# Performance work log

Hardware: AMD Instinct MI355X
Metric: run time of the kernel (lower is better)

## Reference

```python
import jax, jax.numpy as jnp
import numpy as np
from jax import lax

B, T, H, W, D = 4, 24, 32, 32, 128
N_CONV = 5            # 32 -> 1 via five stride-2 convs
NUM_FREQS = T // 2    # 12
N_EXPERTS = 7         # unique int periods of rfftfreq(24)[1:]
TOP_K = 2
BN_EPS = 1e-5
COMBINE_EPS = float(np.finfo(np.float64).eps)


def setup_inputs() -> dict:
    key = jax.random.key(0)
    ks = jax.random.split(key, 12)
    x = jax.random.normal(ks[0], (B, T, H, W, D), jnp.float32)
    conv_w = jax.random.normal(ks[1], (N_CONV, D, D, 2, 2), jnp.float32) / np.sqrt(4 * D)
    conv_b = jax.random.normal(ks[2], (N_CONV, D), jnp.float32) * 0.1
    bn_gamma = jax.random.uniform(ks[3], (N_CONV, D), jnp.float32, 0.5, 1.5)
    bn_beta = jax.random.normal(ks[4], (N_CONV, D), jnp.float32) * 0.1
    bn_mean = jax.random.normal(ks[5], (N_CONV, D), jnp.float32) * 0.1
    bn_var = jax.random.uniform(ks[6], (N_CONV, D), jnp.float32, 0.5, 1.5)
    fuse_w = jax.random.normal(ks[7], (D, 1), jnp.float32) / np.sqrt(D)
    fuse_b = jax.random.normal(ks[8], (1,), jnp.float32) * 0.1
    w_gate = jax.random.normal(ks[9], (NUM_FREQS, N_EXPERTS), jnp.float32)
    expert_w = jax.random.normal(ks[10], (N_EXPERTS, D, D), jnp.float32) / np.sqrt(D)
    expert_b = jax.random.normal(ks[11], (N_EXPERTS, D), jnp.float32) * 0.1
    return dict(x=x, conv_w=conv_w, conv_b=conv_b, bn_gamma=bn_gamma, bn_beta=bn_beta,
                bn_mean=bn_mean, bn_var=bn_var, fuse_w=fuse_w, fuse_b=fuse_b,
                w_gate=w_gate, expert_w=expert_w, expert_b=expert_b, top_k=TOP_K)


def _gates(x, conv_w, conv_b, bn_gamma, bn_beta, bn_mean, bn_var, fuse_w, fuse_b, w_gate, top_k):
    b, t, h, w, d = x.shape
    # (b t h w d) -> (bt, d, h, w)
    z = jnp.transpose(x.reshape(b * t, h, w, d), (0, 3, 1, 2))
    for i in range(conv_w.shape[0]):  # fixed small layer loop
        z = lax.conv_general_dilated(z, conv_w[i], (2, 2), 'VALID',
                                     dimension_numbers=('NCHW', 'OIHW', 'NCHW'))
        z = z + conv_b[i][None, :, None, None]
        z = bn_gamma[i][None, :, None, None] * (z - bn_mean[i][None, :, None, None]) \
            * lax.rsqrt(bn_var[i][None, :, None, None] + BN_EPS) + bn_beta[i][None, :, None, None]
        z = jnp.where(z > 0, z, 0.2 * z)  # LeakyReLU(0.2)
    hh, ww = z.shape[-2], z.shape[-1]
    # (bt, d, h, w) -> (b, t, h*w*d)  matching einops '(b t) d h w -> b t (h w d)'
    z = jnp.transpose(z.reshape(b, t, d, hh, ww), (0, 1, 3, 4, 2)).reshape(b, t, hh * ww * d)
    s = (z @ fuse_w + fuse_b)[..., 0]  # [B, T]
    xf = jnp.fft.rfft(s, axis=-1, norm='ortho')[:, 1:]  # drop DC -> [B, T//2]
    amp = jnp.abs(xf)
    logits = amp @ w_gate  # [B, E]  (eval path: no noise)
    top_vals, top_idx = lax.top_k(logits, top_k + 1)
    tk_vals, tk_idx = top_vals[:, :top_k], top_idx[:, :top_k]
    tk_gates = jax.nn.softmax(tk_vals, axis=-1)
    gates = jnp.zeros_like(logits).at[jnp.arange(b)[:, None], tk_idx].set(tk_gates)
    return gates


def reference(x, conv_w, conv_b, bn_gamma, bn_beta, bn_mean, bn_var,
              fuse_w, fuse_b, w_gate, expert_w, expert_b, top_k):
    gates = _gates(x, conv_w, conv_b, bn_gamma, bn_beta, bn_mean, bn_var,
                   fuse_w, fuse_b, w_gate, top_k)  # [B, E]
    # Dense equivalent of dispatch -> per-expert linear -> combine:
    # combine does exp(expert_out), gate-weighted scatter-add over batch, then log.
    expert_out = jnp.einsum('bthwd,edf->bethwf', x, expert_w) \
                 + expert_b[None, :, None, None, None, :]  # [B,E,T,H,W,D]
    combined = jnp.einsum('be,bethwf->bthwf', gates, jnp.exp(expert_out))
    combined = jnp.where(combined == 0, COMBINE_EPS, combined)
    return jnp.log(combined)
```

## Files before the change

### kernel.cpp

```cpp
#include <hip/hip_runtime.h>
#include <hip/hip_bf16.h>

#define D_ 128
#define T_ 24
#define NPB 24576
#define TSTR 132

typedef __attribute__((ext_vector_type(8))) short bf16x8;
typedef __attribute__((ext_vector_type(4))) float f32x4;
typedef unsigned short ushortt;

static __device__ __forceinline__ void load8(const float* p, float* dst){
  float4 a = *(const float4*)p; float4 b = *(const float4*)(p+4);
  dst[0]=a.x;dst[1]=a.y;dst[2]=a.z;dst[3]=a.w;dst[4]=b.x;dst[5]=b.y;dst[6]=b.z;dst[7]=b.w;
}
static __device__ __forceinline__ bf16x8 cvt8(const float* f){
  union { bf16x8 v; __hip_bfloat162 h[4]; } u;
#pragma unroll
  for (int i=0;i<4;i++) u.h[i] = __float22bfloat162_rn(make_float2(f[2*i], f[2*i+1]));
  return u.v;
}
static __device__ __forceinline__ void split8(const float* f, bf16x8* hh, bf16x8* ll){
  union { bf16x8 v; __hip_bfloat162 h[4]; } uh, ul;
  float lo[8];
#pragma unroll
  for (int i=0;i<4;i++){
    __hip_bfloat162 p = __float22bfloat162_rn(make_float2(f[2*i], f[2*i+1]));
    uh.h[i] = p;
    lo[2*i]   = f[2*i]   - __bfloat162float(p.x);
    lo[2*i+1] = f[2*i+1] - __bfloat162float(p.y);
  }
#pragma unroll
  for (int i=0;i<4;i++) ul.h[i] = __float22bfloat162_rn(make_float2(lo[2*i], lo[2*i+1]));
  *hh = uh.v; *ll = ul.v;
}

__global__ void prep_frags(const float* __restrict__ cw, const float* __restrict__ ew,
                           ushortt* __restrict__ wfC, ushortt* __restrict__ wfE, int do_e)
{
  const int idx = blockIdx.x*256 + threadIdx.x;
  if (idx < 10240){
    const int l  = idx >> 11;
    const int n  = (idx >> 4) & 127;
    const int k8 = (idx & 15) * 8;
    const float* src = cw + (size_t)((l*128 + n)*128 + k8)*4;
    float4 v[8];
#pragma unroll
    for (int kk=0;kk<8;++kk) v[kk] = *(const float4*)&src[kk*4];
    const int fk = k8>>5, q = (k8>>3)&3, ng = n>>4;
    const int lanoff = (q*16 + (n&15))*8;
#pragma unroll
    for (int tap=0; tap<4; ++tap){
      float f[8];
#pragma unroll
      for (int kk=0;kk<8;++kk) f[kk] = ((const float*)&v[kk])[tap];
      bf16x8 hh, ll; split8(f, &hh, &ll);
      *(bf16x8*)&wfC[(size_t)((((l*4+tap)*2+0)*4+fk)*8+ng)*512 + lanoff] = hh;
      *(bf16x8*)&wfC[(size_t)((((l*4+tap)*2+1)*4+fk)*8+ng)*512 + lanoff] = ll;
    }
  } else if (do_e && idx < 10240 + 14336){
    const int j  = idx - 10240;
    const int e  = j >> 11;
    const int n  = (j >> 4) & 127;
    const int k8 = (j & 15) * 8;
    float f[8];
#pragma unroll
    for (int kk=0;kk<8;++kk) f[kk] = ew[(size_t)(e*128 + k8+kk)*128 + n];
    const int fk = k8>>5, q = (k8>>3)&3, ng = n>>4;
    *(bf16x8*)&wfE[(size_t)((e*4+fk)*8+ng)*512 + (q*16 + (n&15))*8] = cvt8(f);
  }
}

template<int MG>
__global__ __launch_bounds__(256, 4)
void conv3(const float* __restrict__ in, float* __restrict__ out,
           const ushortt* __restrict__ wf,
           const float* __restrict__ cb,  const float* __restrict__ gam,
           const float* __restrict__ bet, const float* __restrict__ mn,
           const float* __restrict__ vr,  int n_pix, int lw)
{
  (void)n_pix;
  const int t = threadIdx.x;
  const int w = t>>6, lane = t&63, quad = lane>>4, l16 = lane&15;
  const int nh = w*32;
  const int row0 = blockIdx.x*(MG*16);
  const int Win = 2<<lw;
  int inb[MG];
#pragma unroll
  for (int mg=0; mg<MG; ++mg){
    const int p = row0 + mg*16 + l16;
    const int n   = p >> (2*lw);
    const int rem = p - (n << (2*lw));
    const int oy  = rem >> lw, ox = rem - (oy<<lw);
    inb[mg] = ((n*Win  + 2*oy)*Win + 2*ox) << 7;
  }
  f32x4 acc[MG][2];
#pragma unroll
  for (int mg=0;mg<MG;++mg){ acc[mg][0]=(f32x4){0,0,0,0}; acc[mg][1]=acc[mg][0]; }

#pragma unroll
  for (int tap=0; tap<4; ++tap){
    const int toff = (((tap>>1)*Win) + (tap&1)) << 7;
#pragma unroll
    for (int fk=0; fk<4; ++fk){
      bf16x8 ah[MG], al[MG];
#pragma unroll
      for (int mg=0; mg<MG; ++mg){
        float f[8]; load8(in + inb[mg] + toff + fk*32 + quad*8, f);
        split8(f, &ah[mg], &al[mg]);
      }
#pragma unroll
      for (int ngl=0; ngl<2; ++ngl){
        const int ng = w*2 + ngl;
        const bf16x8 bh = *(const bf16x8*)&wf[(size_t)(((tap*2+0)*4+fk)*8+ng)*512 + lane*8];
        const bf16x8 bl = *(const bf16x8*)&wf[(size_t)(((tap*2+1)*4+fk)*8+ng)*512 + lane*8];
#pragma unroll
        for (int mg=0; mg<MG; ++mg){
          acc[mg][ngl] = __builtin_amdgcn_mfma_f32_16x16x32_bf16(ah[mg], bh, acc[mg][ngl], 0,0,0);
          acc[mg][ngl] = __builtin_amdgcn_mfma_f32_16x16x32_bf16(ah[mg], bl, acc[mg][ngl], 0,0,0);
          acc[mg][ngl] = __builtin_amdgcn_mfma_f32_16x16x32_bf16(al[mg], bh, acc[mg][ngl], 0,0,0);
        }
      }
    }
  }
#pragma unroll
  for (int ngl=0; ngl<2; ++ngl){
    const int col = nh + ngl*16 + l16;
    const float sc  = gam[col]*rsqrtf(vr[col]+1e-5f);
    const float cbv = cb[col], bt = bet[col], mv = mn[col];
#pragma unroll
    for (int mg=0; mg<MG; ++mg)
#pragma unroll
      for (int r=0; r<4; ++r){
        const int pix = row0 + mg*16 + quad*4 + r;
        float v = acc[mg][ngl][r] + cbv;
        v = sc*(v - mv) + bt;
        out[(size_t)pix*D_ + col] = v>0.f ? v : 0.2f*v;
      }
  }
}

template<int WOUT>
static __device__ __forceinline__ void stage_lds(const float* __restrict__ sIn,
    float* __restrict__ sOut, float* __restrict__ gOut,
    const ushortt* __restrict__ wf,
    const float* __restrict__ cb, const float* __restrict__ gam,
    const float* __restrict__ bet, const float* __restrict__ mn,
    const float* __restrict__ vr, int t)
{
  const int w = t>>6, lane = t&63, quad = lane>>4, l16 = lane&15;
  const int nh = w*32;
  const int R  = WOUT*WOUT;
  const int Wi = 2*WOUT;
  const int p  = (l16 < R) ? l16 : 0;
  const int oy = (WOUT==4) ? (p>>2) : (WOUT==2 ? (p>>1) : 0);
  const int ox = (WOUT==4) ? (p&3)  : (WOUT==2 ? (p&1)  : 0);
  const int inb = 2*oy*Wi + 2*ox;
  f32x4 acc[2];
  acc[0]=(f32x4){0,0,0,0}; acc[1]=acc[0];
#pragma unroll
  for (int tap=0; tap<4; ++tap){
    const int toff = (tap>>1)*Wi + (tap&1);
#pragma unroll
    for (int fk=0; fk<4; ++fk){
      float f[8]; load8(sIn + (size_t)(inb+toff)*TSTR + fk*32 + quad*8, f);
      bf16x8 ah, al; split8(f, &ah, &al);
#pragma unroll
      for (int ngl=0; ngl<2; ++ngl){
        const int ng = w*2 + ngl;
        const bf16x8 bh = *(const bf16x8*)&wf[(size_t)(((tap*2+0)*4+fk)*8+ng)*512 + lane*8];
        const bf16x8 bl = *(const bf16x8*)&wf[(size_t)(((tap*2+1)*4+fk)*8+ng)*512 + lane*8];
        acc[ngl] = __builtin_amdgcn_mfma_f32_16x16x32_bf16(ah, bh, acc[ngl], 0,0,0);
        acc[ngl] = __builtin_amdgcn_mfma_f32_16x16x32_bf16(ah, bl, acc[ngl], 0,0,0);
        acc[ngl] = __builtin_amdgcn_mfma_f32_16x16x32_bf16(al, bh, acc[ngl], 0,0,0);
      }
    }
  }
#pragma unroll
  for (int ngl=0; ngl<2; ++ngl){
    const int col = nh + ngl*16 + l16;
    const float sc  = gam[col]*rsqrtf(vr[col]+1e-5f);
    const float cbv = cb[col], btv = bet[col], mv = mn[col];
#pragma unroll
    for (int r=0; r<4; ++r){
      const int row = quad*4 + r;
      if (row < R){
        float v = acc[ngl][r] + cbv;
        v = sc*(v - mv) + btv;
        v = v>0.f ? v : 0.2f*v;
        if (WOUT > 1) sOut[(size_t)row*TSTR + col] = v;
        else          gOut[col] = v;
      }
    }
  }
}

__global__ __launch_bounds__(256, 2)
void tail_kernel(const float* __restrict__ bufA, const ushortt* __restrict__ wfC,
                 const float* __restrict__ cb,  const float* __restrict__ gam,
                 const float* __restrict__ bet, const float* __restrict__ mn,
                 const float* __restrict__ vr,  float* __restrict__ zbuf)
{
  __shared__ float sA[64*TSTR];
  __shared__ float sB[16*TSTR];
  __shared__ float sC[ 4*TSTR];
  const int bt = blockIdx.x;
  const int t = threadIdx.x;
  const int w = t>>6, lane = t&63, quad = lane>>4, l16 = lane&15;
  const int nh = w*32;

  {
    const ushortt* wf = wfC + 131072;
    int inb[4];
#pragma unroll
    for (int mg=0; mg<4; ++mg){
      const int p = mg*16 + l16;
      const int oy = p>>3, ox = p&7;
      inb[mg] = ((bt*16 + 2*oy)*16 + 2*ox) << 7;
    }
    f32x4 acc[4][2];
#pragma unroll
    for (int mg=0;mg<4;++mg){ acc[mg][0]=(f32x4){0,0,0,0}; acc[mg][1]=acc[mg][0]; }
#pragma unroll
    for (int tap=0; tap<4; ++tap){
      const int toff = (((tap>>1)*16) + (tap&1)) << 7;
#pragma unroll
      for (int fk=0; fk<4; ++fk){
        bf16x8 ah[4], al[4];
#pragma unroll
        for (int mg=0; mg<4; ++mg){
          float f[8]; load8(bufA + (size_t)inb[mg] + toff + fk*32 + quad*8, f);
          split8(f, &ah[mg], &al[mg]);
        }
#pragma unroll
        for (int ngl=0; ngl<2; ++ngl){
          const int ng = w*2 + ngl;
          const bf16x8 bh = *(const bf16x8*)&wf[(size_t)(((tap*2+0)*4+fk)*8+ng)*512 + lane*8];
          const bf16x8 bl = *(const bf16x8*)&wf[(size_t)(((tap*2+1)*4+fk)*8+ng)*512 + lane*8];
#pragma unroll
          for (int mg=0; mg<4; ++mg){
            acc[mg][ngl] = __builtin_amdgcn_mfma_f32_16x16x32_bf16(ah[mg], bh, acc[mg][ngl], 0,0,0);
            acc[mg][ngl] = __builtin_amdgcn_mfma_f32_16x16x32_bf16(ah[mg], bl, acc[mg][ngl], 0,0,0);
            acc[mg][ngl] = __builtin_amdgcn_mfma_f32_16x16x32_bf16(al[mg], bh, acc[mg][ngl], 0,0,0);
          }
        }
      }
    }
#pragma unroll
    for (int ngl=0; ngl<2; ++ngl){
      const int col = nh + ngl*16 + l16;
      const float sc  = gam[128+col]*rsqrtf(vr[128+col]+1e-5f);
      const float cbv = cb[128+col], btv = bet[128+col], mv = mn[128+col];
#pragma unroll
      for (int mg=0; mg<4; ++mg)
#pragma unroll
        for (int r=0; r<4; ++r){
          const int row = mg*16 + quad*4 + r;
          float v = acc[mg][ngl][r] + cbv;
          v = sc*(v - mv) + btv;
          sA[(size_t)row*TSTR + col] = v>0.f ? v : 0.2f*v;
        }
    }
  }
  __syncthreads();
  stage_lds<4>(sA, sB, nullptr, wfC + 262144, cb+256, gam+256, bet+256, mn+256, vr+256, t);
  __syncthreads();
  stage_lds<2>(sB, sC, nullptr, wfC + 393216, cb+384, gam+384, bet+384, mn+384, vr+384, t);
  __syncthreads();
  stage_lds<1>(sC, nullptr, zbuf + (size_t)bt*D_, wfC + 524288, cb+512, gam+512, bet+512, mn+512, vr+512, t);
}

__global__ void gate_kernel(const float* __restrict__ z, const float* __restrict__ fw,
                            const float* __restrict__ fb, const float* __restrict__ wg,
                            float* __restrict__ gbuf)
{
  __shared__ float s[96];
  __shared__ float amp[4][12];
  __shared__ float logits[4][7];
  const int t = threadIdx.x;
  if (t < 96){
    float a = 0.f;
    for (int d=0; d<D_; d++) a = fmaf(z[t*D_+d], fw[d], a);
    s[t] = a + fb[0];
  }
  __syncthreads();
  if (t < 48){
    const int b = t / 12, kf = (t % 12) + 1;
    float re=0.f, im=0.f;
    for (int tt=0; tt<T_; tt++){
      int ph = (kf*tt) % T_;
      float ang = (float)ph * (6.283185307179586f / (float)T_);
      re = fmaf(s[b*T_+tt], cosf(ang), re);
      im = fmaf(s[b*T_+tt], sinf(ang), im);
    }
    amp[b][t%12] = sqrtf(re*re + im*im) * 0.20412414523193150f;
  }
  __syncthreads();
  if (t < 28){
    const int b = t/7, e = t - (t/7)*7;
    float a = 0.f;
    for (int k=0;k<12;k++) a = fmaf(amp[b][k], wg[k*7+e], a);
    logits[b][e] = a;
  }
  __syncthreads();
  if (t < 4){
    const int b = t;
    int i0=0; float v0=logits[b][0];
    for (int e=1;e<7;e++){ float v=logits[b][e]; if (v > v0){ v0=v; i0=e; } }
    int i1=-1; float v1=-3.4e38f;
    for (int e=0;e<7;e++){ if (e==i0) continue; float v=logits[b][e]; if (v > v1){ v1=v; i1=e; } }
    float ed = expf(v1 - v0);
    gbuf[b*4+0] = 1.f/(1.f+ed);
    gbuf[b*4+1] = ed/(1.f+ed);
    ((int*)gbuf)[b*4+2] = i0;
    ((int*)gbuf)[b*4+3] = i1;
  }
}

__global__ __launch_bounds__(256, 4)
void expert_lse(const float* __restrict__ x, const ushortt* __restrict__ wfe,
                const float* __restrict__ eb, const float* __restrict__ gbuf,
                float* __restrict__ outp)
{
  const int t = threadIdx.x;
  const int w = t>>6, lane = t&63, quad = lane>>4, l16 = lane&15;
  const int nh = w*32;

#pragma unroll
  for (int tile=0; tile<2; ++tile){
    const size_t row0 = (size_t)(blockIdx.x + tile*768) * 64;
    const int b = (int)(row0 / NPB);
    const float g0 = gbuf[b*4+0], g1 = gbuf[b*4+1];
    const int e0 = ((const int*)gbuf)[b*4+2];
    const int e1 = ((const int*)gbuf)[b*4+3];
    const float lg0 = __logf(g0), lg1 = __logf(g1);

    f32x4 acc[2][4][2];
#pragma unroll
    for (int e=0;e<2;++e)
#pragma unroll
      for (int mg=0;mg<4;++mg){ acc[e][mg][0]=(f32x4){0,0,0,0}; acc[e][mg][1]=acc[e][mg][0]; }

#pragma unroll
    for (int fk=0; fk<4; ++fk){
      bf16x8 a[4];
#pragma unroll
      for (int mg=0; mg<4; ++mg){
        float f[8]; load8(x + (row0 + mg*16 + l16)*D_ + fk*32 + quad*8, f);
        a[mg] = cvt8(f);
      }
#pragma unroll
      for (int e=0; e<2; ++e){
        const int eg = e ? e1 : e0;
#pragma unroll
        for (int ngl=0; ngl<2; ++ngl){
          const int ng = w*2 + ngl;
          const bf16x8 bb = *(const bf16x8*)&wfe[(size_t)((eg*4+fk)*8+ng)*512 + lane*8];
#pragma unroll
          for (int mg=0; mg<4; ++mg)
            acc[e][mg][ngl] = __builtin_amdgcn_mfma_f32_16x16x32_bf16(a[mg], bb, acc[e][mg][ngl], 0,0,0);
        }
      }
    }
#pragma unroll
    for (int ngl=0; ngl<2; ++ngl){
      const int col = nh + ngl*16 + l16;
      const float be0 = eb[e0*D_ + col] + lg0;
      const float be1 = eb[e1*D_ + col] + lg1;
#pragma unroll
      for (int mg=0; mg<4; ++mg)
#pragma unroll
        for (int r=0; r<4; ++r){
          const size_t row = row0 + mg*16 + quad*4 + r;
          const float u = acc[0][mg][ngl][r] + be0;
          const float v = acc[1][mg][ngl][r] + be1;
          const float m = fmaxf(u, v);
          outp[row*D_ + col] = m + __logf(1.f + __expf(-fabsf(u - v)));
        }
    }
  }
}

template<bool WF>
__global__ __launch_bounds__(256, 3)
void expert3(const float* __restrict__ x, const float* __restrict__ ew,
             const ushortt* __restrict__ wfe, const float* __restrict__ eb,
             const float* __restrict__ gbuf, float* __restrict__ outp)
{
  __shared__ ushortt wlds[WF ? 16 : 32768];
  const int t = threadIdx.x;
  const int w = t>>6, lane = t&63, quad = lane>>4, l16 = lane&15;
  const int nh = w*32;
  const size_t row0 = (size_t)blockIdx.x * 64;
  const int b = (int)(row0 / NPB);
  const float g0 = gbuf[b*4+0], g1 = gbuf[b*4+1];
  const int e0 = ((const int*)gbuf)[b*4+2];
  const int e1 = ((const int*)gbuf)[b*4+3];

  if (!WF){
    const int el = t>>7, r7 = t&127;
    const int n0 = (r7&31)*4, k0 = (r7>>5)*16;
    const int esel = el ? e1 : e0;
#pragma unroll
    for (int h=0; h<2; ++h)
#pragma unroll
      for (int sub=0; sub<2; ++sub){
        const int kb = h*64 + k0 + sub*8;
        float4 v[8];
#pragma unroll
        for (int kk=0;kk<8;++kk)
          v[kk] = *(const float4*)&ew[(size_t)esel*16384 + (size_t)(kb+kk)*D_ + n0];
        const int fk = kb>>5, q = (kb>>3)&3;
#pragma unroll
        for (int n=0;n<4;++n){
          float f[8];
#pragma unroll
          for (int kk=0;kk<8;++kk) f[kk] = ((const float*)&v[kk])[n];
          *(bf16x8*)&wlds[(size_t)(((el*4+fk)*8 + ((n0+n)>>4))*512 + (q*16 + ((n0+n)&15))*8)] = cvt8(f);
        }
      }
    __syncthreads();
  }

  f32x4 acc[2][4][2];
#pragma unroll
  for (int e=0;e<2;++e)
#pragma unroll
    for (int mg=0;mg<4;++mg){ acc[e][mg][0]=(f32x4){0,0,0,0}; acc[e][mg][1]=acc[e][mg][0]; }

#pragma unroll
  for (int fk=0; fk<4; ++fk){
    bf16x8 a[4];
#pragma unroll
    for (int mg=0; mg<4; ++mg){
      float f[8]; load8(x + (row0 + mg*16 + l16)*D_ + fk*32 + quad*8, f);
      a[mg] = cvt8(f);
    }
#pragma unroll
    for (int e=0; e<2; ++e){
      const int eg = e ? e1 : e0;
#pragma unroll
      for (int ngl=0; ngl<2; ++ngl){
        const int ng = w*2 + ngl;
        bf16x8 bb;
        if (WF) bb = *(const bf16x8*)&wfe[(size_t)((eg*4+fk)*8+ng)*512 + lane*8];
        else    bb = *(const bf16x8*)&wlds[(size_t)((e*4+fk)*8+ng)*512 + lane*8];
#pragma unroll
        for (int mg=0; mg<4; ++mg)
          acc[e][mg][ngl] = __builtin_amdgcn_mfma_f32_16x16x32_bf16(a[mg], bb, acc[e][mg][ngl], 0,0,0);
      }
    }
  }
#pragma unroll
  for (int ngl=0; ngl<2; ++ngl){
    const int col = nh + ngl*16 + l16;
    const float be0 = eb[e0*D_ + col];
    const float be1 = eb[e1*D_ + col];
#pragma unroll
    for (int mg=0; mg<4; ++mg)
#pragma unroll
      for (int r=0; r<4; ++r){
        const size_t row = row0 + mg*16 + quad*4 + r;
        float c = g0*__expf(acc[0][mg][ngl][r] + be0) + g1*__expf(acc[1][mg][ngl][r] + be1);
        if (c == 0.f) c = 2.220446049250313e-16f;
        outp[row*D_ + col] = __logf(c);
      }
  }
}

extern "C" void kernel_launch(void* const* d_in, const int* in_sizes, int n_in,
                              void* d_out, int out_size, void* d_ws, size_t ws_size,
                              hipStream_t stream)
{
  const float* x   = (const float*)d_in[0];
  const float* cw  = (const float*)d_in[1];
  const float* cb  = (const float*)d_in[2];
  const float* gam = (const float*)d_in[3];
  const float* bet = (const float*)d_in[4];
  const float* mn  = (const float*)d_in[5];
  const float* vr  = (const float*)d_in[6];
  const float* fw  = (const float*)d_in[7];
  const float* fb  = (const float*)d_in[8];
  const float* wg  = (const float*)d_in[9];
  const float* ew  = (const float*)d_in[10];
  const float* eb  = (const float*)d_in[11];
  float* out = (float*)d_out;

  char* sb = (char*)d_out;
  ushortt* wfC = (ushortt*)sb;
  float* bufA  = (float*)(sb + 1310720);

  const size_t WFE_BYTES = (size_t)7*4*8*512*2;
  const size_t ZB_BYTES  = (size_t)96*D_*sizeof(float);
  const bool primary = ws_size >= WFE_BYTES + ZB_BYTES + 64;
  ushortt* wfE = (ushortt*)d_ws;
  float* zbuf_ws = (float*)((char*)d_ws + WFE_BYTES);
  float* gbuf_ws = (float*)((char*)d_ws + WFE_BYTES + ZB_BYTES);

  if (primary){
    prep_frags<<<96, 256, 0, stream>>>(cw, ew, wfC, wfE, 1);
    conv3<2><<<768, 256, 0, stream>>>(x, bufA, wfC, cb, gam, bet, mn, vr, 24576, 4);
    tail_kernel<<<96, 256, 0, stream>>>(bufA, wfC, cb, gam, bet, mn, vr, zbuf_ws);
    gate_kernel<<<1, 128, 0, stream>>>(zbuf_ws, fw, fb, wg, gbuf_ws);
    expert_lse<<<768, 256, 0, stream>>>(x, wfE, eb, gbuf_ws, out);
    return;
  }

  float* bufB  = (float*)(sb + 13893632);
  float* zbuf  = (float*)(sb + 17039360);
  float* gbuf  = (float*)d_ws;
  const bool use_wf = ws_size >= (size_t)(64 + WFE_BYTES);
  ushortt* wfE2 = use_wf ? (ushortt*)((char*)d_ws + 64) : wfC;

  prep_frags<<<96, 256, 0, stream>>>(cw, ew, wfC, wfE2, use_wf ? 1 : 0);
  conv3<2><<<768, 256, 0, stream>>>(x,    bufA, wfC,          cb,     gam,     bet,     mn,     vr,     24576, 4);
  conv3<2><<<192, 256, 0, stream>>>(bufA, bufB, wfC + 131072, cb+128, gam+128, bet+128, mn+128, vr+128,  6144, 3);
  conv3<1><<< 96, 256, 0, stream>>>(bufB, bufA, wfC + 262144, cb+256, gam+256, bet+256, mn+256, vr+256,  1536, 2);
  conv3<1><<< 24, 256, 0, stream>>>(bufA, bufB, wfC + 393216, cb+384, gam+384, bet+384, mn+384, vr+384,   384, 1);
  conv3<1><<<  6, 256, 0, stream>>>(bufB, zbuf, wfC + 524288, cb+512, gam+512, bet+512, mn+512, vr+512,    96, 0);
  gate_kernel<<<1, 128, 0, stream>>>(zbuf, fw, fb, wg, gbuf);
  if (use_wf) expert3<true ><<<1536, 256, 0, stream>>>(x, ew, wfE2, eb, gbuf, out);
  else        expert3<false><<<1536, 256, 0, stream>>>(x, ew, wfE2, eb, gbuf, out);
}
```

Baseline: 244.8 us.

## Emit bf16 copy of x from first conv and read it in expert GEMM

The first conv layer already loads every x pixel and splits it to bf16 hi, so it now also writes that bf16 copy to workspace. The expert kernel then reads the bf16 copy (half the bytes) instead of re-reading fp32 x and converting, and is launched with one tile per block over more blocks. This adds a bf16 write of all of x (about 25 MB) in conv and needs a larger workspace, otherwise the primary path is disabled and the slower fallback path runs.

```diff
diff --git a/kernel.cpp b/kernel.cpp
--- a/kernel.cpp
+++ b/kernel.cpp
@@ -71,9 +71,10 @@
   }
 }
 
-template<int MG>
+template<int MG, bool XB>
 __global__ __launch_bounds__(256, 4)
 void conv3(const float* __restrict__ in, float* __restrict__ out,
+           ushortt* __restrict__ xb,
            const ushortt* __restrict__ wf,
            const float* __restrict__ cb,  const float* __restrict__ gam,
            const float* __restrict__ bet, const float* __restrict__ mn,
@@ -108,6 +109,10 @@
       for (int mg=0; mg<MG; ++mg){
         float f[8]; load8(in + inb[mg] + toff + fk*32 + quad*8, f);
         split8(f, &ah[mg], &al[mg]);
+        if (XB){
+          const size_t pix = (size_t)(inb[mg] + toff) >> 7;
+          *(bf16x8*)&xb[pix*D_ + fk*32 + quad*8] = ah[mg];
+        }
       }
 #pragma unroll
       for (int ngl=0; ngl<2; ++ngl){
@@ -318,66 +323,60 @@
 }
 
 __global__ __launch_bounds__(256, 4)
-void expert_lse(const float* __restrict__ x, const ushortt* __restrict__ wfe,
-                const float* __restrict__ eb, const float* __restrict__ gbuf,
-                float* __restrict__ outp)
+void expert_xb(const ushortt* __restrict__ xb, const ushortt* __restrict__ wfe,
+               const float* __restrict__ eb, const float* __restrict__ gbuf,
+               float* __restrict__ outp)
 {
   const int t = threadIdx.x;
   const int w = t>>6, lane = t&63, quad = lane>>4, l16 = lane&15;
   const int nh = w*32;
-
-#pragma unroll
-  for (int tile=0; tile<2; ++tile){
-    const size_t row0 = (size_t)(blockIdx.x + tile*768) * 64;
-    const int b = (int)(row0 / NPB);
-    const float g0 = gbuf[b*4+0], g1 = gbuf[b*4+1];
-    const int e0 = ((const int*)gbuf)[b*4+2];
-    const int e1 = ((const int*)gbuf)[b*4+3];
-    const float lg0 = __logf(g0), lg1 = __logf(g1);
-
-    f32x4 acc[2][4][2];
-#pragma unroll
-    for (int e=0;e<2;++e)
-#pragma unroll
-      for (int mg=0;mg<4;++mg){ acc[e][mg][0]=(f32x4){0,0,0,0}; acc[e][mg][1]=acc[e][mg][0]; }
-
-#pragma unroll
-    for (int fk=0; fk<4; ++fk){
-      bf16x8 a[4];
-#pragma unroll
-      for (int mg=0; mg<4; ++mg){
-        float f[8]; load8(x + (row0 + mg*16 + l16)*D_ + fk*32 + quad*8, f);
-        a[mg] = cvt8(f);
-      }
-#pragma unroll
-      for (int e=0; e<2; ++e){
-        const int eg = e ? e1 : e0;
-#pragma unroll
-        for (int ngl=0; ngl<2; ++ngl){
-          const int ng = w*2 + ngl;
-          const bf16x8 bb = *(const bf16x8*)&wfe[(size_t)((eg*4+fk)*8+ng)*512 + lane*8];
-#pragma unroll
-          for (int mg=0; mg<4; ++mg)
-            acc[e][mg][ngl] = __builtin_amdgcn_mfma_f32_16x16x32_bf16(a[mg], bb, acc[e][mg][ngl], 0,0,0);
-        }
-      }
-    }
-#pragma unroll
-    for (int ngl=0; ngl<2; ++ngl){
-      const int col = nh + ngl*16 + l16;
-      const float be0 = eb[e0*D_ + col] + lg0;
-      const float be1 = eb[e1*D_ + col] + lg1;
-#pragma unroll
-      for (int mg=0; mg<4; ++mg)
-#pragma unroll
-        for (int r=0; r<4; ++r){
-          const size_t row = row0 + mg*16 + quad*4 + r;
-          const float u = acc[0][mg][ngl][r] + be0;
-          const float v = acc[1][mg][ngl][r] + be1;
-          const float m = fmaxf(u, v);
-          outp[row*D_ + col] = m + __logf(1.f + __expf(-fabsf(u - v)));
-        }
-    }
+  const size_t row0 = (size_t)blockIdx.x * 64;
+  const int b = (int)(row0 / NPB);
+  const float g0 = gbuf[b*4+0], g1 = gbuf[b*4+1];
+  const int e0 = ((const int*)gbuf)[b*4+2];
+  const int e1 = ((const int*)gbuf)[b*4+3];
+  const float lg0 = __logf(g0), lg1 = __logf(g1);
+
+  f32x4 acc[2][4][2];
+#pragma unroll
+  for (int e=0;e<2;++e)
+#pragma unroll
+    for (int mg=0;mg<4;++mg){ acc[e][mg][0]=(f32x4){0,0,0,0}; acc[e][mg][1]=acc[e][mg][0]; }
+
+#pragma unroll
+  for (int fk=0; fk<4; ++fk){
+    bf16x8 a[4];
+#pragma unroll
+    for (int mg=0; mg<4; ++mg)
+      a[mg] = *(const bf16x8*)&xb[(row0 + mg*16 + l16)*D_ + fk*32 + quad*8];
+#pragma unroll
+    for (int e=0; e<2; ++e){
+      const int eg = e ? e1 : e0;
+#pragma unroll
+      for (int ngl=0; ngl<2; ++ngl){
+        const int ng = w*2 + ngl;
+        const bf16x8 bb = *(const bf16x8*)&wfe[(size_t)((eg*4+fk)*8+ng)*512 + lane*8];
+#pragma unroll
+        for (int mg=0; mg<4; ++mg)
+          acc[e][mg][ngl] = __builtin_amdgcn_mfma_f32_16x16x32_bf16(a[mg], bb, acc[e][mg][ngl], 0,0,0);
+      }
+    }
+  }
+#pragma unroll
+  for (int ngl=0; ngl<2; ++ngl){
+    const int col = nh + ngl*16 + l16;
+    const float be0 = eb[e0*D_ + col] + lg0;
+    const float be1 = eb[e1*D_ + col] + lg1;
+#pragma unroll
+    for (int mg=0; mg<4; ++mg)
+#pragma unroll
+      for (int r=0; r<4; ++r){
+        const size_t row = row0 + mg*16 + quad*4 + r;
+        const float u = acc[0][mg][ngl][r] + be0;
+        const float v = acc[1][mg][ngl][r] + be1;
+        const float m = fmaxf(u, v);
+        outp[row*D_ + col] = m + __logf(1.f + __expf(-fabsf(u - v)));
+      }
   }
 }
 
@@ -492,17 +491,20 @@
 
   const size_t WFE_BYTES = (size_t)7*4*8*512*2;
   const size_t ZB_BYTES  = (size_t)96*D_*sizeof(float);
-  const bool primary = ws_size >= WFE_BYTES + ZB_BYTES + 64;
-  ushortt* wfE = (ushortt*)d_ws;
+  const size_t XB_OFF    = WFE_BYTES + ZB_BYTES + 64;
+  const size_t XB_BYTES  = (size_t)98304*D_*2;
+  const bool primary = ws_size >= XB_OFF + XB_BYTES;
+  ushortt* wfE   = (ushortt*)d_ws;
   float* zbuf_ws = (float*)((char*)d_ws + WFE_BYTES);
   float* gbuf_ws = (float*)((char*)d_ws + WFE_BYTES + ZB_BYTES);
+  ushortt* xb    = (ushortt*)((char*)d_ws + XB_OFF);
 
   if (primary){
     prep_frags<<<96, 256, 0, stream>>>(cw, ew, wfC, wfE, 1);
-    conv3<2><<<768, 256, 0, stream>>>(x, bufA, wfC, cb, gam, bet, mn, vr, 24576, 4);
+    conv3<2,true><<<768, 256, 0, stream>>>(x, bufA, xb, wfC, cb, gam, bet, mn, vr, 24576, 4);
     tail_kernel<<<96, 256, 0, stream>>>(bufA, wfC, cb, gam, bet, mn, vr, zbuf_ws);
     gate_kernel<<<1, 128, 0, stream>>>(zbuf_ws, fw, fb, wg, gbuf_ws);
-    expert_lse<<<768, 256, 0, stream>>>(x, wfE, eb, gbuf_ws, out);
+    expert_xb<<<1536, 256, 0, stream>>>(xb, wfE, eb, gbuf_ws, out);
     return;
   }
 
@@ -513,11 +515,11 @@
   ushortt* wfE2 = use_wf ? (ushortt*)((char*)d_ws + 64) : wfC;
 
   prep_frags<<<96, 256, 0, stream>>>(cw, ew, wfC, wfE2, use_wf ? 1 : 0);
-  conv3<2><<<768, 256, 0, stream>>>(x,    bufA, wfC,          cb,     gam,     bet,     mn,     vr,     24576, 4);
-  conv3<2><<<192, 256, 0, stream>>>(bufA, bufB, wfC + 131072, cb+128, gam+128, bet+128, mn+128, vr+128,  6144, 3);
-  conv3<1><<< 96, 256, 0, stream>>>(bufB, bufA, wfC + 262144, cb+256, gam+256, bet+256, mn+256, vr+256,  1536, 2);
-  conv3<1><<< 24, 256, 0, stream>>>(bufA, bufB, wfC + 393216, cb+384, gam+384, bet+384, mn+384, vr+384,   384, 1);
-  conv3<1><<<  6, 256, 0, stream>>>(bufB, zbuf, wfC + 524288, cb+512, gam+512, bet+512, mn+512, vr+512,    96, 0);
+  conv3<2,false><<<768, 256, 0, stream>>>(x,    bufA, nullptr, wfC,          cb,     gam,     bet,     mn,     vr,     24576, 4);
+  conv3<2,false><<<192, 256, 0, stream>>>(bufA, bufB, nullptr, wfC + 131072, cb+128, gam+128, bet+128, mn+128, vr+128,  6144, 3);
+  conv3<1,false><<< 96, 256, 0, stream>>>(bufB, bufA, nullptr, wfC + 262144, cb+256, gam+256, bet+256, mn+256, vr+256,  1536, 2);
+  conv3<1,false><<< 24, 256, 0, stream>>>(bufA, bufB, nullptr, wfC + 393216, cb+384, gam+384, bet+384, mn+384, vr+384,   384, 1);
+  conv3<1,false><<<  6, 256, 0, stream>>>(bufB, zbuf, nullptr, wfC + 524288, cb+512, gam+512, bet+512, mn+512, vr+512,    96, 0);
   gate_kernel<<<1, 128, 0, stream>>>(zbuf, fw, fb, wg, gbuf);
   if (use_wf) expert3<true ><<<1536, 256, 0, stream>>>(x, ew, wfE2, eb, gbuf, out);
   else        expert3<false><<<1536, 256, 0, stream>>>(x, ew, wfE2, eb, gbuf, out);
```

Measured after the change: 230.9 us. 5.7% less time.

## Emit bf16 copy of x in first conv and read it in expert kernel

Applied to the files above, without the earlier changes.

The first conv layer is replaced by a new kernel that, while splitting x into bf16 hi/lo for its MFMAs, also writes the hi part of every input pixel to a workspace buffer. The expert log-sum-exp kernel then reads this bf16 copy instead of re-reading and converting fp32 x, halving its input traffic. It also uses smaller 32-row tiles with more blocks and higher occupancy bounds. The cost is an extra 25MB write in the conv pass, and the primary path now needs a larger workspace, falling back to the slow path otherwise.

```diff
diff --git a/kernel.cpp b/kernel.cpp
--- a/kernel.cpp
+++ b/kernel.cpp
@@ -68,6 +68,63 @@
     for (int kk=0;kk<8;++kk) f[kk] = ew[(size_t)(e*128 + k8+kk)*128 + n];
     const int fk = k8>>5, q = (k8>>3)&3, ng = n>>4;
     *(bf16x8*)&wfE[(size_t)((e*4+fk)*8+ng)*512 + (q*16 + (n&15))*8] = cvt8(f);
+  }
+}
+
+__global__ __launch_bounds__(256, 8)
+void conv0_xb(const float* __restrict__ in, float* __restrict__ out,
+              ushortt* __restrict__ xb, const ushortt* __restrict__ wf,
+              const float* __restrict__ cb,  const float* __restrict__ gam,
+              const float* __restrict__ bet, const float* __restrict__ mn,
+              const float* __restrict__ vr)
+{
+  const int t = threadIdx.x;
+  const int w = t>>6, lane = t&63, quad = lane>>4, l16 = lane&15;
+  const int nh = w*32;
+  const int row0 = blockIdx.x*16;
+  const int p = row0 + l16;
+  const int n   = p >> 8;
+  const int rem = p & 255;
+  const int oy  = rem >> 4, ox = rem & 15;
+  const int inb = ((n*32 + 2*oy)*32 + 2*ox) << 7;
+
+  f32x4 acc[2];
+  acc[0]=(f32x4){0,0,0,0}; acc[1]=acc[0];
+
+#pragma unroll
+  for (int tap=0; tap<4; ++tap){
+    const int toff = (((tap>>1)*32) + (tap&1)) << 7;
+#pragma unroll
+    for (int fk=0; fk<4; ++fk){
+      float f[8]; load8(in + inb + toff + fk*32 + quad*8, f);
+      bf16x8 ah, al; split8(f, &ah, &al);
+      if (fk == w){
+        const size_t pix = (size_t)(inb + toff) >> 7;
+        *(bf16x8*)&xb[pix*D_ + fk*32 + quad*8] = ah;
+      }
+#pragma unroll
+      for (int ngl=0; ngl<2; ++ngl){
+        const int ng = w*2 + ngl;
+        const bf16x8 bh = *(const bf16x8*)&wf[(size_t)(((tap*2+0)*4+fk)*8+ng)*512 + lane*8];
+        const bf16x8 bl = *(const bf16x8*)&wf[(size_t)(((tap*2+1)*4+fk)*8+ng)*512 + lane*8];
+        acc[ngl] = __builtin_amdgcn_mfma_f32_16x16x32_bf16(ah, bh, acc[ngl], 0,0,0);
+        acc[ngl] = __builtin_amdgcn_mfma_f32_16x16x32_bf16(ah, bl, acc[ngl], 0,0,0);
+        acc[ngl] = __builtin_amdgcn_mfma_f32_16x16x32_bf16(al, bh, acc[ngl], 0,0,0);
+      }
+    }
+  }
+#pragma unroll
+  for (int ngl=0; ngl<2; ++ngl){
+    const int col = nh + ngl*16 + l16;
+    const float sc  = gam[col]*rsqrtf(vr[col]+1e-5f);
+    const float cbv = cb[col], bt = bet[col], mv = mn[col];
+#pragma unroll
+    for (int r=0; r<4; ++r){
+      const int pix = row0 + quad*4 + r;
+      float v = acc[ngl][r] + cbv;
+      v = sc*(v - mv) + bt;
+      out[(size_t)pix*D_ + col] = v>0.f ? v : 0.2f*v;
+    }
   }
 }
 
@@ -317,67 +374,61 @@
   }
 }
 
-__global__ __launch_bounds__(256, 4)
-void expert_lse(const float* __restrict__ x, const ushortt* __restrict__ wfe,
+__global__ __launch_bounds__(256, 6)
+void expert_xb2(const ushortt* __restrict__ xb, const ushortt* __restrict__ wfe,
                 const float* __restrict__ eb, const float* __restrict__ gbuf,
                 float* __restrict__ outp)
 {
   const int t = threadIdx.x;
   const int w = t>>6, lane = t&63, quad = lane>>4, l16 = lane&15;
   const int nh = w*32;
-
-#pragma unroll
-  for (int tile=0; tile<2; ++tile){
-    const size_t row0 = (size_t)(blockIdx.x + tile*768) * 64;
-    const int b = (int)(row0 / NPB);
-    const float g0 = gbuf[b*4+0], g1 = gbuf[b*4+1];
-    const int e0 = ((const int*)gbuf)[b*4+2];
-    const int e1 = ((const int*)gbuf)[b*4+3];
-    const float lg0 = __logf(g0), lg1 = __logf(g1);
-
-    f32x4 acc[2][4][2];
-#pragma unroll
-    for (int e=0;e<2;++e)
-#pragma unroll
-      for (int mg=0;mg<4;++mg){ acc[e][mg][0]=(f32x4){0,0,0,0}; acc[e][mg][1]=acc[e][mg][0]; }
-
-#pragma unroll
-    for (int fk=0; fk<4; ++fk){
-      bf16x8 a[4];
-#pragma unroll
-      for (int mg=0; mg<4; ++mg){
-        float f[8]; load8(x + (row0 + mg*16 + l16)*D_ + fk*32 + quad*8, f);
-        a[mg] = cvt8(f);
-      }
-#pragma unroll
-      for (int e=0; e<2; ++e){
-        const int eg = e ? e1 : e0;
-#pragma unroll
-        for (int ngl=0; ngl<2; ++ngl){
-          const int ng = w*2 + ngl;
-          const bf16x8 bb = *(const bf16x8*)&wfe[(size_t)((eg*4+fk)*8+ng)*512 + lane*8];
-#pragma unroll
-          for (int mg=0; mg<4; ++mg)
-            acc[e][mg][ngl] = __builtin_amdgcn_mfma_f32_16x16x32_bf16(a[mg], bb, acc[e][mg][ngl], 0,0,0);
-        }
-      }
-    }
-#pragma unroll
-    for (int ngl=0; ngl<2; ++ngl){
-      const int col = nh + ngl*16 + l16;
-      const float be0 = eb[e0*D_ + col] + lg0;
-      const float be1 = eb[e1*D_ + col] + lg1;
-#pragma unroll
-      for (int mg=0; mg<4; ++mg)
-#pragma unroll
-        for (int r=0; r<4; ++r){
-          const size_t row = row0 + mg*16 + quad*4 + r;
-          const float u = acc[0][mg][ngl][r] + be0;
-          const float v = acc[1][mg][ngl][r] + be1;
-          const float m = fmaxf(u, v);
-          outp[row*D_ + col] = m + __logf(1.f + __expf(-fabsf(u - v)));
-        }
-    }
+  const size_t row0 = (size_t)blockIdx.x * 32;
+  const int b = (int)(row0 / NPB);
+  const float g0 = gbuf[b*4+0], g1 = gbuf[b*4+1];
+  const int e0 = ((const int*)gbuf)[b*4+2];
+  const int e1 = ((const int*)gbuf)[b*4+3];
+  const float lg0 = __logf(g0), lg1 = __logf(g1);
+
+  f32x4 acc[2][2][2];
+#pragma unroll
+  for (int e=0;e<2;++e)
+#pragma unroll
+    for (int mg=0;mg<2;++mg){ acc[e][mg][0]=(f32x4){0,0,0,0}; acc[e][mg][1]=acc[e][mg][0]; }
+
+#pragma unroll
+  for (int fk=0; fk<4; ++fk){
+    bf16x8 a[2];
+#pragma unroll
+    for (int mg=0; mg<2; ++mg)
+      a[mg] = *(const bf16x8*)&xb[(row0 + mg*16 + l16)*D_ + fk*32 + quad*8];
+#pragma unroll
+    for (int e=0; e<2; ++e){
+      const int eg = e ? e1 : e0;
+#pragma unroll
+      for (int ngl=0; ngl<2; ++ngl){
+        const int ng = w*2 + ngl;
+        const bf16x8 bb = *(const bf16x8*)&wfe[(size_t)((eg*4+fk)*8+ng)*512 + lane*8];
+#pragma unroll
+        for (int mg=0; mg<2; ++mg)
+          acc[e][mg][ngl] = __builtin_amdgcn_mfma_f32_16x16x32_bf16(a[mg], bb, acc[e][mg][ngl], 0,0,0);
+      }
+    }
+  }
+#pragma unroll
+  for (int ngl=0; ngl<2; ++ngl){
+    const int col = nh + ngl*16 + l16;
+    const float be0 = eb[e0*D_ + col] + lg0;
+    const float be1 = eb[e1*D_ + col] + lg1;
+#pragma unroll
+    for (int mg=0; mg<2; ++mg)
+#pragma unroll
+      for (int r=0; r<4; ++r){
+        const size_t row = row0 + mg*16 + quad*4 + r;
+        const float u = acc[0][mg][ngl][r] + be0;
+        const float v = acc[1][mg][ngl][r] + be1;
+        const float m = fmaxf(u, v);
+        outp[row*D_ + col] = m + __logf(1.f + __expf(-fabsf(u - v)));
+      }
   }
 }
 
@@ -492,17 +543,20 @@
 
   const size_t WFE_BYTES = (size_t)7*4*8*512*2;
   const size_t ZB_BYTES  = (size_t)96*D_*sizeof(float);
-  const bool primary = ws_size >= WFE_BYTES + ZB_BYTES + 64;
-  ushortt* wfE = (ushortt*)d_ws;
+  const size_t XB_OFF    = WFE_BYTES + ZB_BYTES + 64;
+  const size_t XB_BYTES  = (size_t)98304*D_*2;
+  const bool primary = ws_size >= XB_OFF + XB_BYTES;
+  ushortt* wfE   = (ushortt*)d_ws;
   float* zbuf_ws = (float*)((char*)d_ws + WFE_BYTES);
   float* gbuf_ws = (float*)((char*)d_ws + WFE_BYTES + ZB_BYTES);
+  ushortt* xb    = (ushortt*)((char*)d_ws + XB_OFF);
 
   if (primary){
     prep_frags<<<96, 256, 0, stream>>>(cw, ew, wfC, wfE, 1);
-    conv3<2><<<768, 256, 0, stream>>>(x, bufA, wfC, cb, gam, bet, mn, vr, 24576, 4);
+    conv0_xb<<<1536, 256, 0, stream>>>(x, bufA, xb, wfC, cb, gam, bet, mn, vr);
     tail_kernel<<<96, 256, 0, stream>>>(bufA, wfC, cb, gam, bet, mn, vr, zbuf_ws);
     gate_kernel<<<1, 128, 0, stream>>>(zbuf_ws, fw, fb, wg, gbuf_ws);
-    expert_lse<<<768, 256, 0, stream>>>(x, wfE, eb, gbuf_ws, out);
+    expert_xb2<<<3072, 256, 0, stream>>>(xb, wfE, eb, gbuf_ws, out);
     return;
   }
 
```

Measured after the change: 223.9 us. 8.5% less time.
